# Optimization experiments

Measured on AMD Instinct MI355X. Metric: run time of the kernel, lower is better.

Reference implementation:

```python
import jax, jax.numpy as jnp
import numpy as np

B, N, M = 2048, 4096, 4096


def setup_inputs() -> dict:
    key = jax.random.key(0)
    kt, kv, kr = jax.random.split(key, 3)
    # sorted abscissae per sample (interp1d assumes monotone t)
    t = jnp.sort(jax.random.uniform(kt, (B, N), dtype=jnp.float32), axis=-1)
    v = jax.random.normal(kv, (B, N), dtype=jnp.float32)
    # queries slightly outside [0,1] to exercise the extrapolation clamp
    r = jax.random.uniform(kr, (B, M), minval=-0.05, maxval=1.05, dtype=jnp.float32)
    return {"t": t, "v": v, "r": r}


def _interp1(t, v, r):
    # t: [N] sorted, v: [N], r: [M]
    idx = jnp.clip(jnp.searchsorted(t, r, side='right'), 1, t.shape[0] - 1)
    t0 = t[idx - 1]
    t1 = t[idx]
    v0 = v[idx - 1]
    v1 = v[idx]
    denom = jnp.where(t1 == t0, jnp.float32(1.0), t1 - t0)
    out = v0 + (r - t0) / denom * (v1 - v0)
    # scipy fill_value=(v[0], v[-1]) with bounds_error=False: clamp extrapolation
    out = jnp.where(r < t[0], v[0], out)
    out = jnp.where(r > t[-1], v[-1], out)
    return out


def reference(t, v, r):
    # batched 1D linear interpolation with clamped extrapolation -> [B, M]
    return jax.vmap(_interp1)(t, v, r)
```

## Files before the change

kernel.cpp:

```cpp
#include <hip/hip_runtime.h>
#include <float.h>

constexpr int B = 2048;
constexpr int N = 4096;
constexpr int M = 4096;
constexpr int K = 4072;
constexpr int T = 512;

__global__ __launch_bounds__(T, 8) void interp_kernel(
    const float* __restrict__ t,
    const float* __restrict__ v,
    const float* __restrict__ r,
    float* __restrict__ out) {
    __shared__ __align__(16) float st[N + 8];
    __shared__ __align__(16) float sv[N + 4];
    __shared__ unsigned short lut[K];

    const int tid = threadIdx.x;
    const int b = blockIdx.x;
    const float* tb = t + (size_t)b * N;
    const float* vb = v + (size_t)b * N;
    const float4* r4 = (const float4*)(r + (size_t)b * M);
    float4* o4 = (float4*)(out + (size_t)b * M);

    const float4 t4a = ((const float4*)tb)[tid];
    const float4 t4b = ((const float4*)tb)[tid + T];
    const float4 v4a = ((const float4*)vb)[tid];
    const float4 v4b = ((const float4*)vb)[tid + T];
    const float4 qa = r4[tid];
    const float4 qb = r4[tid + T];

    if (tid < 8) st[N + tid] = FLT_MAX;
    if (tid < 4) sv[N + tid] = 0.0f;

    ((float4*)st)[tid]     = t4a;
    ((float4*)st)[tid + T] = t4b;
    ((float4*)sv)[tid]     = v4a;
    ((float4*)sv)[tid + T] = v4b;

    {
        float tpa = __shfl_up(t4a.w, 1);
        if ((tid & 63) == 0 && tid > 0) tpa = tb[4 * tid - 1];
        float tpb = __shfl_up(t4b.w, 1);
        if ((tid & 63) == 0) tpb = tb[4 * (tid + T) - 1];
        const float pe[8] = {tpa, t4a.x, t4a.y, t4a.z, tpb, t4b.x, t4b.y, t4b.z};
        const float ce[8] = {t4a.x, t4a.y, t4a.z, t4a.w, t4b.x, t4b.y, t4b.z, t4b.w};
        #pragma unroll
        for (int e = 0; e < 8; ++e) {
            const int j = (e < 4 ? 4 * tid : 4 * (tid + T)) + (e & 3);
            int khi = (int)(ce[e] * (float)K);
            khi = khi > K - 1 ? K - 1 : khi;
            if (j == N - 1) khi = K - 1;
            const int klo = (j == 0) ? 0 : (int)(pe[e] * (float)K) + 1;
            for (int k = klo; k <= khi; ++k) lut[k] = (unsigned short)j;
        }
    }
    __syncthreads();

    const float tfirst = st[0];
    const float vfirst = sv[0];
    const float tlast = st[N - 1];
    const float vlast = sv[N - 1];

    const float q[8] = {qa.x, qa.y, qa.z, qa.w, qb.x, qb.y, qb.z, qb.w};
    int bs[8];
    float a0[8], a1[8], a2[8], a3[8];
    float tt0[8], tt1[8];
    int idx[8];
    float v0[8], v1[8];
    float o[8];

    #pragma unroll
    for (int j = 0; j < 8; ++j) {
        int k = (int)(q[j] * (float)K);
        k = k < 0 ? 0 : (k > K - 1 ? K - 1 : k);
        int lo = lut[k];
        lo = lo < 1 ? 1 : lo;
        bs[j] = lo - 1;
    }
    #pragma unroll
    for (int j = 0; j < 8; ++j) {
        a0[j] = st[bs[j] + 0];
        a1[j] = st[bs[j] + 1];
        a2[j] = st[bs[j] + 2];
        a3[j] = st[bs[j] + 3];
    }
    #pragma unroll
    for (int j = 0; j < 8; ++j) {
        int c = (a0[j] <= q[j] ? 1 : 0) + (a1[j] <= q[j] ? 1 : 0) +
                (a2[j] <= q[j] ? 1 : 0) + (a3[j] <= q[j] ? 1 : 0);
        c = c < 1 ? 1 : c;
        float t0 = (c >= 2) ? ((c >= 3) ? a2[j] : a1[j]) : a0[j];
        float t1 = (c >= 2) ? ((c >= 3) ? a3[j] : a2[j]) : a1[j];
        int ix = bs[j] + c;
        if (c == 4) {
            float tp = a3[j];
            int l = bs[j] + 4;
            float tc = st[l];
            while (tc <= q[j]) { tp = tc; ++l; tc = st[l]; }
            t0 = tp; t1 = tc; ix = l;
        }
        tt0[j] = t0; tt1[j] = t1; idx[j] = ix;
    }
    #pragma unroll
    for (int j = 0; j < 8; ++j) {
        v0[j] = sv[idx[j] - 1];
        v1[j] = sv[idx[j]];
    }
    #pragma unroll
    for (int j = 0; j < 8; ++j) {
        const float d = tt1[j] - tt0[j];
        const float rden = __builtin_amdgcn_rcpf(d == 0.0f ? 1.0f : d);
        float oo = v0[j] + (q[j] - tt0[j]) * rden * (v1[j] - v0[j]);
        oo = (q[j] < tfirst) ? vfirst : oo;
        oo = (q[j] > tlast) ? vlast : oo;
        o[j] = oo;
    }
    o4[tid]     = make_float4(o[0], o[1], o[2], o[3]);
    o4[tid + T] = make_float4(o[4], o[5], o[6], o[7]);
}

extern "C" void kernel_launch(void* const* d_in, const int* in_sizes, int n_in,
                              void* d_out, int out_size, void* d_ws, size_t ws_size,
                              hipStream_t stream) {
    const float* t = (const float*)d_in[0];
    const float* v = (const float*)d_in[1];
    const float* r = (const float*)d_in[2];
    float* out = (float*)d_out;
    interp_kernel<<<B, T, 0, stream>>>(t, v, r, out);
}
```

Baseline: 135.3 us.

## Interleave t and v in shared memory and enlarge lookup table

Stores t and v as interleaved float2 pairs so one aligned 32-byte window read gives both abscissae and values. This removes the second dependent LDS gather for v0/v1. The LUT grows to 12288 entries so each bucket covers fewer points, making the scan-fallback loop rarer. In exchange, LDS use per block rises to about 57KB, so the launch bounds drop to 4 blocks/SM, reducing occupancy. The window is also aligned down to an even index, so it may cover fewer points ahead of the LUT index.

```diff
diff --git a/kernel.cpp b/kernel.cpp
--- a/kernel.cpp
+++ b/kernel.cpp
@@ -4,16 +4,15 @@
 constexpr int B = 2048;
 constexpr int N = 4096;
 constexpr int M = 4096;
-constexpr int K = 4072;
+constexpr int K = 12288;
 constexpr int T = 512;
 
-__global__ __launch_bounds__(T, 8) void interp_kernel(
+__global__ __launch_bounds__(T, 4) void interp_kernel(
     const float* __restrict__ t,
     const float* __restrict__ v,
     const float* __restrict__ r,
     float* __restrict__ out) {
-    __shared__ __align__(16) float st[N + 8];
-    __shared__ __align__(16) float sv[N + 4];
+    __shared__ __align__(16) float2 stv[N + 8];
     __shared__ unsigned short lut[K];
 
     const int tid = threadIdx.x;
@@ -30,13 +29,15 @@
     const float4 qa = r4[tid];
     const float4 qb = r4[tid + T];
 
-    if (tid < 8) st[N + tid] = FLT_MAX;
-    if (tid < 4) sv[N + tid] = 0.0f;
+    if (tid < 8) stv[N + tid] = make_float2(FLT_MAX, 0.0f);
 
-    ((float4*)st)[tid]     = t4a;
-    ((float4*)st)[tid + T] = t4b;
-    ((float4*)sv)[tid]     = v4a;
-    ((float4*)sv)[tid + T] = v4b;
+    {
+        float4* s4 = (float4*)stv;
+        s4[2 * tid + 0]       = make_float4(t4a.x, v4a.x, t4a.y, v4a.y);
+        s4[2 * tid + 1]       = make_float4(t4a.z, v4a.z, t4a.w, v4a.w);
+        s4[2 * (tid + T) + 0] = make_float4(t4b.x, v4b.x, t4b.y, v4b.y);
+        s4[2 * (tid + T) + 1] = make_float4(t4b.z, v4b.z, t4b.w, v4b.w);
+    }
 
     {
         float tpa = __shfl_up(t4a.w, 1);
@@ -57,17 +58,14 @@
     }
     __syncthreads();
 
-    const float tfirst = st[0];
-    const float vfirst = sv[0];
-    const float tlast = st[N - 1];
-    const float vlast = sv[N - 1];
+    const float tfirst = stv[0].x;
+    const float vfirst = stv[0].y;
+    const float tlast = stv[N - 1].x;
+    const float vlast = stv[N - 1].y;
 
     const float q[8] = {qa.x, qa.y, qa.z, qa.w, qb.x, qb.y, qb.z, qb.w};
-    int bs[8];
-    float a0[8], a1[8], a2[8], a3[8];
-    float tt0[8], tt1[8];
-    int idx[8];
-    float v0[8], v1[8];
+    int b2[8];
+    float4 wA[8], wB[8];
     float o[8];
 
     #pragma unroll
@@ -76,42 +74,34 @@
         k = k < 0 ? 0 : (k > K - 1 ? K - 1 : k);
         int lo = lut[k];
         lo = lo < 1 ? 1 : lo;
-        bs[j] = lo - 1;
+        b2[j] = (lo - 1) & ~1;
     }
     #pragma unroll
     for (int j = 0; j < 8; ++j) {
-        a0[j] = st[bs[j] + 0];
-        a1[j] = st[bs[j] + 1];
-        a2[j] = st[bs[j] + 2];
-        a3[j] = st[bs[j] + 3];
+        const float4* w4 = (const float4*)(stv + b2[j]);
+        wA[j] = w4[0];
+        wB[j] = w4[1];
     }
     #pragma unroll
     for (int j = 0; j < 8; ++j) {
-        int c = (a0[j] <= q[j] ? 1 : 0) + (a1[j] <= q[j] ? 1 : 0) +
-                (a2[j] <= q[j] ? 1 : 0) + (a3[j] <= q[j] ? 1 : 0);
+        const float ta0 = wA[j].x, ta1 = wA[j].z, ta2 = wB[j].x, ta3 = wB[j].z;
+        int c = (ta0 <= q[j] ? 1 : 0) + (ta1 <= q[j] ? 1 : 0) +
+                (ta2 <= q[j] ? 1 : 0) + (ta3 <= q[j] ? 1 : 0);
         c = c < 1 ? 1 : c;
-        float t0 = (c >= 2) ? ((c >= 3) ? a2[j] : a1[j]) : a0[j];
-        float t1 = (c >= 2) ? ((c >= 3) ? a3[j] : a2[j]) : a1[j];
-        int ix = bs[j] + c;
+        float t0 = (c >= 2) ? ((c >= 3) ? ta2 : ta1) : ta0;
+        float t1 = (c >= 2) ? ((c >= 3) ? ta3 : ta2) : ta1;
+        float v0 = (c >= 2) ? ((c >= 3) ? wB[j].y : wA[j].w) : wA[j].y;
+        float v1 = (c >= 2) ? ((c >= 3) ? wB[j].w : wB[j].y) : wA[j].w;
         if (c == 4) {
-            float tp = a3[j];
-            int l = bs[j] + 4;
-            float tc = st[l];
-            while (tc <= q[j]) { tp = tc; ++l; tc = st[l]; }
-            t0 = tp; t1 = tc; ix = l;
+            float tp = ta3, vp = wB[j].w;
+            int l = b2[j] + 4;
+            float2 cur = stv[l];
+            while (cur.x <= q[j]) { tp = cur.x; vp = cur.y; ++l; cur = stv[l]; }
+            t0 = tp; t1 = cur.x; v0 = vp; v1 = cur.y;
         }
-        tt0[j] = t0; tt1[j] = t1; idx[j] = ix;
-    }
-    #pragma unroll
-    for (int j = 0; j < 8; ++j) {
-        v0[j] = sv[idx[j] - 1];
-        v1[j] = sv[idx[j]];
-    }
-    #pragma unroll
-    for (int j = 0; j < 8; ++j) {
-        const float d = tt1[j] - tt0[j];
+        const float d = t1 - t0;
         const float rden = __builtin_amdgcn_rcpf(d == 0.0f ? 1.0f : d);
-        float oo = v0[j] + (q[j] - tt0[j]) * rden * (v1[j] - v0[j]);
+        float oo = v0 + (q[j] - t0) * rden * (v1 - v0);
         oo = (q[j] < tfirst) ? vfirst : oo;
         oo = (q[j] > tlast) ? vlast : oo;
         o[j] = oo;
```

Result: slower. 143.1 us (+5.8%).

## Drop shared-memory staging of values and triple lookup table resolution

Applied to the files above, without the earlier changes.

Removes the shared-memory copy of v and gathers the two interpolation values straight from global memory (through cache) at the found index. Only the boundary values are loaded up front. The freed LDS is spent on a larger lookup table, so the initial guess lands closer and fewer fallback linear-scan steps are needed. The cost is scattered global gathers in place of LDS reads, plus a larger LUT fill per block, which may reduce occupancy.

```diff
diff --git a/kernel.cpp b/kernel.cpp
--- a/kernel.cpp
+++ b/kernel.cpp
@@ -4,7 +4,7 @@
 constexpr int B = 2048;
 constexpr int N = 4096;
 constexpr int M = 4096;
-constexpr int K = 4072;
+constexpr int K = 12256;
 constexpr int T = 512;
 
 __global__ __launch_bounds__(T, 8) void interp_kernel(
@@ -13,7 +13,6 @@
     const float* __restrict__ r,
     float* __restrict__ out) {
     __shared__ __align__(16) float st[N + 8];
-    __shared__ __align__(16) float sv[N + 4];
     __shared__ unsigned short lut[K];
 
     const int tid = threadIdx.x;
@@ -25,18 +24,14 @@
 
     const float4 t4a = ((const float4*)tb)[tid];
     const float4 t4b = ((const float4*)tb)[tid + T];
-    const float4 v4a = ((const float4*)vb)[tid];
-    const float4 v4b = ((const float4*)vb)[tid + T];
     const float4 qa = r4[tid];
     const float4 qb = r4[tid + T];
+    const float vfirst = vb[0];
+    const float vlast = vb[N - 1];
 
     if (tid < 8) st[N + tid] = FLT_MAX;
-    if (tid < 4) sv[N + tid] = 0.0f;
-
     ((float4*)st)[tid]     = t4a;
     ((float4*)st)[tid + T] = t4b;
-    ((float4*)sv)[tid]     = v4a;
-    ((float4*)sv)[tid + T] = v4b;
 
     {
         float tpa = __shfl_up(t4a.w, 1);
@@ -58,54 +53,52 @@
     __syncthreads();
 
     const float tfirst = st[0];
-    const float vfirst = sv[0];
     const float tlast = st[N - 1];
-    const float vlast = sv[N - 1];
 
     const float q[8] = {qa.x, qa.y, qa.z, qa.w, qb.x, qb.y, qb.z, qb.w};
-    int bs[8];
-    float a0[8], a1[8], a2[8], a3[8];
+    int lo[8];
+    float w0[8], w1[8], w2[8], w3[8];
     float tt0[8], tt1[8];
     int idx[8];
-    float v0[8], v1[8];
     float o[8];
 
     #pragma unroll
     for (int j = 0; j < 8; ++j) {
         int k = (int)(q[j] * (float)K);
         k = k < 0 ? 0 : (k > K - 1 ? K - 1 : k);
-        int lo = lut[k];
-        lo = lo < 1 ? 1 : lo;
-        bs[j] = lo - 1;
+        int l = lut[k];
+        lo[j] = l < 1 ? 1 : l;
     }
     #pragma unroll
     for (int j = 0; j < 8; ++j) {
-        a0[j] = st[bs[j] + 0];
-        a1[j] = st[bs[j] + 1];
-        a2[j] = st[bs[j] + 2];
-        a3[j] = st[bs[j] + 3];
+        w0[j] = st[lo[j] - 1];
+        w1[j] = st[lo[j] + 0];
+        w2[j] = st[lo[j] + 1];
+        w3[j] = st[lo[j] + 2];
     }
     #pragma unroll
     for (int j = 0; j < 8; ++j) {
-        int c = (a0[j] <= q[j] ? 1 : 0) + (a1[j] <= q[j] ? 1 : 0) +
-                (a2[j] <= q[j] ? 1 : 0) + (a3[j] <= q[j] ? 1 : 0);
+        int c = (w0[j] <= q[j] ? 1 : 0) + (w1[j] <= q[j] ? 1 : 0) +
+                (w2[j] <= q[j] ? 1 : 0) + (w3[j] <= q[j] ? 1 : 0);
         c = c < 1 ? 1 : c;
-        float t0 = (c >= 2) ? ((c >= 3) ? a2[j] : a1[j]) : a0[j];
-        float t1 = (c >= 2) ? ((c >= 3) ? a3[j] : a2[j]) : a1[j];
-        int ix = bs[j] + c;
+        float t0 = (c == 1) ? w0[j] : ((c == 2) ? w1[j] : w2[j]);
+        float t1 = (c == 1) ? w1[j] : ((c == 2) ? w2[j] : w3[j]);
+        int ix = lo[j] - 1 + c;
         if (c == 4) {
-            float tp = a3[j];
-            int l = bs[j] + 4;
+            float tp = w3[j];
+            int l = lo[j] + 3;
             float tc = st[l];
             while (tc <= q[j]) { tp = tc; ++l; tc = st[l]; }
             t0 = tp; t1 = tc; ix = l;
         }
         tt0[j] = t0; tt1[j] = t1; idx[j] = ix;
     }
+    float v0[8], v1[8];
     #pragma unroll
     for (int j = 0; j < 8; ++j) {
-        v0[j] = sv[idx[j] - 1];
-        v1[j] = sv[idx[j]];
+        const int i1 = idx[j] > N - 1 ? N - 1 : idx[j];
+        v0[j] = vb[idx[j] - 1];
+        v1[j] = vb[i1];
     }
     #pragma unroll
     for (int j = 0; j < 8; ++j) {
```

New measurement: 142.9 us. 1.06x slower.
